# Optimization experiments

Measured on AMD Instinct MI355X. Metric: run time of the kernel, lower is better.

## Reference

```python
import jax, jax.numpy as jnp
import numpy as np

B, F, D = 16384, 40, 64  # batch, num_fields, embedding_size
D_OUT = 64               # att_embedding_size * head_num = 32 * 2


def setup_inputs() -> dict:
    key = jax.random.key(0)
    ks = jax.random.split(key, 5)
    return {
        "inputs": jax.random.normal(ks[0], (B, F, D), dtype=jnp.float32),
        "W_Query": jax.random.normal(ks[1], (D, D_OUT), dtype=jnp.float32) * 0.05,
        "W_key": jax.random.normal(ks[2], (D, D_OUT), dtype=jnp.float32) * 0.05,
        "W_Value": jax.random.normal(ks[3], (D, D_OUT), dtype=jnp.float32) * 0.05,
        "W_Res": jax.random.normal(ks[4], (D, D_OUT), dtype=jnp.float32) * 0.05,
    }


def reference(inputs, W_Query, W_key, W_Value, W_Res):
    # QKV projections (no head splitting, per original module)
    q = jnp.einsum('bfd,de->bfe', inputs, W_Query)  # [B, F, D_OUT]
    k = jnp.einsum('bfd,de->bfe', inputs, W_key)
    v = jnp.einsum('bfd,de->bfe', inputs, W_Value)
    # scaled-dot-product over the field axis; scaling=False so no divide
    scores = jax.nn.softmax(jnp.einsum('bqe,bke->bqk', q, k), axis=-1)  # [B, F, F]
    result = jnp.einsum('bqk,bke->bqe', scores, v)
    # residual projection (use_res=True)
    result = result + jnp.einsum('bfd,de->bfe', inputs, W_Res)
    return jax.nn.relu(result)
```

## Files before the change

kernel.cpp:

```cpp
#include <hip/hip_runtime.h>
#include <hip/hip_bf16.h>

#define BB  16384
#define F   40
#define LDQ 72
#define LDV 56

typedef __bf16 bf16;
typedef __bf16 bf16x8 __attribute__((ext_vector_type(8)));
typedef __bf16 bf16x4 __attribute__((ext_vector_type(4)));
typedef float  f32x4  __attribute__((ext_vector_type(4)));


__device__ __forceinline__ bf16x8 cvt8(float4 a, float4 b) {
    bf16x8 f;
    f[0] = (bf16)a.x; f[1] = (bf16)a.y; f[2] = (bf16)a.z; f[3] = (bf16)a.w;
    f[4] = (bf16)b.x; f[5] = (bf16)b.y; f[6] = (bf16)b.z; f[7] = (bf16)b.w;
    return f;
}

__global__ __launch_bounds__(256)
void prep_weights(const float* __restrict__ Wq, const float* __restrict__ Wk,
                  const float* __restrict__ Wv, const float* __restrict__ Wr,
                  bf16* __restrict__ ws)
{
    const int tid = threadIdx.x;
    if (blockIdx.x > 0) {
        const float* W = (blockIdx.x == 1) ? Wv : Wr;
        bf16* dst = ws + 4096 * blockIdx.x;
        for (int f = tid; f < 4096; f += 256) {
            int j = f & 7, ln = (f >> 3) & 63, kt = (f >> 9) & 1, nt = f >> 10;
            dst[f] = (bf16)W[(kt * 32 + (ln >> 4) * 8 + j) * 64 + nt * 16 + (ln & 15)];
        }
        return;
    }
    __shared__ float Gs[64 * 64];
    if (tid < 64) {
        const int l16 = tid & 15, quad = tid >> 4;
        bf16x8 aq[4][2], ak[4][2];
        #pragma unroll
        for (int mt = 0; mt < 4; ++mt)
            #pragma unroll
            for (int kt = 0; kt < 2; ++kt) {
                const float* pq = Wq + (mt * 16 + l16) * 64 + kt * 32 + quad * 8;
                const float* pk = Wk + (mt * 16 + l16) * 64 + kt * 32 + quad * 8;
                aq[mt][kt] = cvt8(*(const float4*)pq, *(const float4*)(pq + 4));
                ak[mt][kt] = cvt8(*(const float4*)pk, *(const float4*)(pk + 4));
            }
        #pragma unroll
        for (int mt = 0; mt < 4; ++mt)
            #pragma unroll
            for (int nt = 0; nt < 4; ++nt) {
                f32x4 acc = {0.f, 0.f, 0.f, 0.f};
                acc = __builtin_amdgcn_mfma_f32_16x16x32_bf16(aq[mt][0], ak[nt][0], acc, 0, 0, 0);
                acc = __builtin_amdgcn_mfma_f32_16x16x32_bf16(aq[mt][1], ak[nt][1], acc, 0, 0, 0);
                #pragma unroll
                for (int r = 0; r < 4; ++r)
                    Gs[(mt * 16 + quad * 4 + r) * 64 + nt * 16 + l16] = acc[r];
            }
    }
    __syncthreads();
    for (int f = tid; f < 4096; f += 256) {
        int j = f & 7, ln = (f >> 3) & 63, kt = (f >> 9) & 1, nt = f >> 10;
        ws[f] = (bf16)Gs[(kt * 32 + (ln >> 4) * 8 + j) * 64 + nt * 16 + (ln & 15)];
    }
}

__global__ __launch_bounds__(64, 3)
void attn_fused(const float* __restrict__ X, const bf16* __restrict__ wfrag,
                float* __restrict__ Out)
{
    __shared__ bf16 QB[48 * LDQ];
    __shared__ bf16 VT[64 * LDV + 8];

    const int lane = threadIdx.x;
    const int l16  = lane & 15;
    const int quad = lane >> 4;
    const int b    = blockIdx.x;
    const float* Xb = X + (size_t)b * (F * 64);

    {
        bf16x8 z = {};
        *(bf16x8*)&VT[lane * LDV + 48] = z;
        if (lane == 0) *(bf16x8*)&VT[64 * LDV] = z;
    }

    bf16x8 xf[3][2];
    #pragma unroll
    for (int mt = 0; mt < 3; ++mt) {
        int row = mt * 16 + l16; if (row >= F) row = F - 1;
        #pragma unroll
        for (int kt = 0; kt < 2; ++kt) {
            const float* p = Xb + row * 64 + kt * 32 + quad * 8;
            xf[mt][kt] = cvt8(*(const float4*)p, *(const float4*)(p + 4));
        }
    }

    const bf16x8* gF = (const bf16x8*)wfrag;
    const bf16x8* vF = gF + 512;
    const bf16x8* rF = gF + 1024;

    #pragma unroll
    for (int mt = 0; mt < 4; ++mt) {
        bf16x8 a0 = gF[(mt * 2 + 0) * 64 + lane];
        bf16x8 a1 = gF[(mt * 2 + 1) * 64 + lane];
        #pragma unroll
        for (int nt = 0; nt < 3; ++nt) {
            f32x4 acc = {0.f, 0.f, 0.f, 0.f};
            acc = __builtin_amdgcn_mfma_f32_16x16x32_bf16(a0, xf[nt][0], acc, 0, 0, 0);
            acc = __builtin_amdgcn_mfma_f32_16x16x32_bf16(a1, xf[nt][1], acc, 0, 0, 0);
            bf16x4 pk;
            pk[0] = (bf16)acc[0]; pk[1] = (bf16)acc[1];
            pk[2] = (bf16)acc[2]; pk[3] = (bf16)acc[3];
            *(bf16x4*)&QB[(nt * 16 + l16) * LDQ + mt * 16 + quad * 4] = pk;
        }
    }

    #pragma unroll
    for (int nt = 0; nt < 4; ++nt) {
        bf16x8 b0 = vF[(nt * 2 + 0) * 64 + lane];
        bf16x8 b1 = vF[(nt * 2 + 1) * 64 + lane];
        #pragma unroll
        for (int mt = 0; mt < 3; ++mt) {
            f32x4 acc = {0.f, 0.f, 0.f, 0.f};
            acc = __builtin_amdgcn_mfma_f32_16x16x32_bf16(xf[mt][0], b0, acc, 0, 0, 0);
            acc = __builtin_amdgcn_mfma_f32_16x16x32_bf16(xf[mt][1], b1, acc, 0, 0, 0);
            bf16x4 pk;
            pk[0] = (bf16)acc[0]; pk[1] = (bf16)acc[1];
            pk[2] = (bf16)acc[2]; pk[3] = (bf16)acc[3];
            *(bf16x4*)&VT[(nt * 16 + l16) * LDV + mt * 16 + quad * 4] = pk;
        }
    }

    bf16x8 qf[3][2];
    #pragma unroll
    for (int nt = 0; nt < 3; ++nt) {
        qf[nt][0] = *(const bf16x8*)&QB[(nt * 16 + l16) * LDQ + 0  + quad * 8];
        qf[nt][1] = *(const bf16x8*)&QB[(nt * 16 + l16) * LDQ + 32 + quad * 8];
    }
    f32x4 sacc[3][3];
    #pragma unroll
    for (int mt = 0; mt < 3; ++mt)
        #pragma unroll
        for (int nt = 0; nt < 3; ++nt) {
            f32x4 acc = {0.f, 0.f, 0.f, 0.f};
            acc = __builtin_amdgcn_mfma_f32_16x16x32_bf16(xf[mt][0], qf[nt][0], acc, 0, 0, 0);
            acc = __builtin_amdgcn_mfma_f32_16x16x32_bf16(xf[mt][1], qf[nt][1], acc, 0, 0, 0);
            sacc[mt][nt] = acc;
        }

    const bool dead = (quad >= 2);
    #pragma unroll
    for (int nt = 0; nt < 3; ++nt) {
        float ex[3][4]; float sum = 0.f;
        #pragma unroll
        for (int mt = 0; mt < 3; ++mt)
            #pragma unroll
            for (int r = 0; r < 4; ++r) {
                float e = (mt == 2 && dead) ? 0.f : __expf(sacc[mt][nt][r]);
                ex[mt][r] = e; sum += e;
            }
        sum += __shfl_xor(sum, 16, 64);
        sum += __shfl_xor(sum, 32, 64);
        float inv = 1.0f / sum;
        #pragma unroll
        for (int mt = 0; mt < 3; ++mt) {
            bf16x4 pk;
            pk[0] = (bf16)(ex[mt][0] * inv); pk[1] = (bf16)(ex[mt][1] * inv);
            pk[2] = (bf16)(ex[mt][2] * inv); pk[3] = (bf16)(ex[mt][3] * inv);
            *(bf16x4*)&QB[(nt * 16 + l16) * LDQ + mt * 16 + quad * 4] = pk;
        }
    }

    f32x4 oacc[4][3];
    #pragma unroll
    for (int mt = 0; mt < 4; ++mt) {
        bf16x8 a0 = rF[(mt * 2 + 0) * 64 + lane];
        bf16x8 a1 = rF[(mt * 2 + 1) * 64 + lane];
        #pragma unroll
        for (int nt = 0; nt < 3; ++nt) {
            f32x4 acc = {0.f, 0.f, 0.f, 0.f};
            acc = __builtin_amdgcn_mfma_f32_16x16x32_bf16(a0, xf[nt][0], acc, 0, 0, 0);
            acc = __builtin_amdgcn_mfma_f32_16x16x32_bf16(a1, xf[nt][1], acc, 0, 0, 0);
            oacc[mt][nt] = acc;
        }
    }
    bf16x8 ptf[3][2];
    #pragma unroll
    for (int nt = 0; nt < 3; ++nt) {
        ptf[nt][0] = *(const bf16x8*)&QB[(nt * 16 + l16) * LDQ + 0  + quad * 8];
        bf16x8 t   = *(const bf16x8*)&QB[(nt * 16 + l16) * LDQ + 32 + quad * 8];
        if (dead) t = bf16x8{};
        ptf[nt][1] = t;
    }
    #pragma unroll
    for (int mt = 0; mt < 4; ++mt) {
        bf16x8 v0 = *(const bf16x8*)&VT[(mt * 16 + l16) * LDV + 0  + quad * 8];
        bf16x8 v1 = *(const bf16x8*)&VT[(mt * 16 + l16) * LDV + 32 + quad * 8];
        #pragma unroll
        for (int nt = 0; nt < 3; ++nt) {
            f32x4 acc = oacc[mt][nt];
            acc = __builtin_amdgcn_mfma_f32_16x16x32_bf16(v0, ptf[nt][0], acc, 0, 0, 0);
            acc = __builtin_amdgcn_mfma_f32_16x16x32_bf16(v1, ptf[nt][1], acc, 0, 0, 0);
            int m = nt * 16 + l16;
            if (m < F) {
                f32x4 st;
                st[0] = fmaxf(acc[0], 0.f); st[1] = fmaxf(acc[1], 0.f);
                st[2] = fmaxf(acc[2], 0.f); st[3] = fmaxf(acc[3], 0.f);
                __builtin_nontemporal_store(st,
                    (f32x4*)&Out[(size_t)b * (F * 64) + m * 64 + mt * 16 + quad * 4]);
            }
        }
    }
}

extern "C" void kernel_launch(void* const* d_in, const int* in_sizes, int n_in,
                              void* d_out, int out_size, void* d_ws, size_t ws_size,
                              hipStream_t stream) {
    const float* X  = (const float*)d_in[0];
    const float* Wq = (const float*)d_in[1];
    const float* Wk = (const float*)d_in[2];
    const float* Wv = (const float*)d_in[3];
    const float* Wr = (const float*)d_in[4];
    float* Out = (float*)d_out;
    bf16* ws = (bf16*)d_ws;

    prep_weights<<<3, 256, 0, stream>>>(Wq, Wk, Wv, Wr, ws);
    attn_fused<<<BB, 64, 0, stream>>>(X, ws, Out);
}
```

Measured before the change: 314.2 us.

## Process four batches per block with register prefetch of next X tile

Each single-wave block now loops over four batch elements instead of one, and grid size shrinks accordingly. While the current batch is computed, the fp32 X rows for the next batch are loaded into registers so global load latency overlaps the MFMA work. The output stores are regrouped after the final accumulation. This adds register pressure from the prefetch buffer and cuts the number of blocks available to hide latency through occupancy.

```diff
diff --git a/kernel.cpp b/kernel.cpp
--- a/kernel.cpp
+++ b/kernel.cpp
@@ -3,6 +3,7 @@
 
 #define BB  16384
 #define F   40
+#define NB  4
 #define LDQ 72
 #define LDV 56
 
@@ -76,8 +77,26 @@
     const int lane = threadIdx.x;
     const int l16  = lane & 15;
     const int quad = lane >> 4;
-    const int b    = blockIdx.x;
-    const float* Xb = X + (size_t)b * (F * 64);
+    const long b0  = (long)blockIdx.x * NB;
+
+    int rowm[3];
+    #pragma unroll
+    for (int mt = 0; mt < 3; ++mt) {
+        int r = mt * 16 + l16; rowm[mt] = (r >= F) ? (F - 1) : r;
+    }
+
+    float4 xr[3][2][2];
+    {
+        const float* Xb = X + (size_t)b0 * (F * 64);
+        #pragma unroll
+        for (int mt = 0; mt < 3; ++mt)
+            #pragma unroll
+            for (int kt = 0; kt < 2; ++kt) {
+                const float* p = Xb + rowm[mt] * 64 + kt * 32 + quad * 8;
+                xr[mt][kt][0] = *(const float4*)p;
+                xr[mt][kt][1] = *(const float4*)(p + 4);
+            }
+    }
 
     {
         bf16x8 z = {};
@@ -85,130 +104,152 @@
         if (lane == 0) *(bf16x8*)&VT[64 * LDV] = z;
     }
 
-    bf16x8 xf[3][2];
-    #pragma unroll
-    for (int mt = 0; mt < 3; ++mt) {
-        int row = mt * 16 + l16; if (row >= F) row = F - 1;
-        #pragma unroll
-        for (int kt = 0; kt < 2; ++kt) {
-            const float* p = Xb + row * 64 + kt * 32 + quad * 8;
-            xf[mt][kt] = cvt8(*(const float4*)p, *(const float4*)(p + 4));
-        }
-    }
-
-    const bf16x8* gF = (const bf16x8*)wfrag;
-    const bf16x8* vF = gF + 512;
-    const bf16x8* rF = gF + 1024;
-
-    #pragma unroll
-    for (int mt = 0; mt < 4; ++mt) {
-        bf16x8 a0 = gF[(mt * 2 + 0) * 64 + lane];
-        bf16x8 a1 = gF[(mt * 2 + 1) * 64 + lane];
-        #pragma unroll
-        for (int nt = 0; nt < 3; ++nt) {
-            f32x4 acc = {0.f, 0.f, 0.f, 0.f};
-            acc = __builtin_amdgcn_mfma_f32_16x16x32_bf16(a0, xf[nt][0], acc, 0, 0, 0);
-            acc = __builtin_amdgcn_mfma_f32_16x16x32_bf16(a1, xf[nt][1], acc, 0, 0, 0);
-            bf16x4 pk;
-            pk[0] = (bf16)acc[0]; pk[1] = (bf16)acc[1];
-            pk[2] = (bf16)acc[2]; pk[3] = (bf16)acc[3];
-            *(bf16x4*)&QB[(nt * 16 + l16) * LDQ + mt * 16 + quad * 4] = pk;
-        }
-    }
-
-    #pragma unroll
-    for (int nt = 0; nt < 4; ++nt) {
-        bf16x8 b0 = vF[(nt * 2 + 0) * 64 + lane];
-        bf16x8 b1 = vF[(nt * 2 + 1) * 64 + lane];
-        #pragma unroll
-        for (int mt = 0; mt < 3; ++mt) {
-            f32x4 acc = {0.f, 0.f, 0.f, 0.f};
-            acc = __builtin_amdgcn_mfma_f32_16x16x32_bf16(xf[mt][0], b0, acc, 0, 0, 0);
-            acc = __builtin_amdgcn_mfma_f32_16x16x32_bf16(xf[mt][1], b1, acc, 0, 0, 0);
-            bf16x4 pk;
-            pk[0] = (bf16)acc[0]; pk[1] = (bf16)acc[1];
-            pk[2] = (bf16)acc[2]; pk[3] = (bf16)acc[3];
-            *(bf16x4*)&VT[(nt * 16 + l16) * LDV + mt * 16 + quad * 4] = pk;
-        }
-    }
-
-    bf16x8 qf[3][2];
-    #pragma unroll
-    for (int nt = 0; nt < 3; ++nt) {
-        qf[nt][0] = *(const bf16x8*)&QB[(nt * 16 + l16) * LDQ + 0  + quad * 8];
-        qf[nt][1] = *(const bf16x8*)&QB[(nt * 16 + l16) * LDQ + 32 + quad * 8];
-    }
-    f32x4 sacc[3][3];
-    #pragma unroll
-    for (int mt = 0; mt < 3; ++mt)
-        #pragma unroll
-        for (int nt = 0; nt < 3; ++nt) {
-            f32x4 acc = {0.f, 0.f, 0.f, 0.f};
-            acc = __builtin_amdgcn_mfma_f32_16x16x32_bf16(xf[mt][0], qf[nt][0], acc, 0, 0, 0);
-            acc = __builtin_amdgcn_mfma_f32_16x16x32_bf16(xf[mt][1], qf[nt][1], acc, 0, 0, 0);
-            sacc[mt][nt] = acc;
-        }
-
-    const bool dead = (quad >= 2);
-    #pragma unroll
-    for (int nt = 0; nt < 3; ++nt) {
-        float ex[3][4]; float sum = 0.f;
+    const bf16* wf = wfrag;
+
+    #pragma unroll 1
+    for (int i = 0; i < NB; ++i) {
+        const long b = b0 + i;
+
+        asm volatile("" : "+s"(wf));
+        const bf16x8* gF = (const bf16x8*)wf;
+        const bf16x8* vF = gF + 512;
+        const bf16x8* rF = gF + 1024;
+
+        bf16x8 xf[3][2];
         #pragma unroll
         for (int mt = 0; mt < 3; ++mt)
             #pragma unroll
-            for (int r = 0; r < 4; ++r) {
-                float e = (mt == 2 && dead) ? 0.f : __expf(sacc[mt][nt][r]);
-                ex[mt][r] = e; sum += e;
-            }
-        sum += __shfl_xor(sum, 16, 64);
-        sum += __shfl_xor(sum, 32, 64);
-        float inv = 1.0f / sum;
-        #pragma unroll
-        for (int mt = 0; mt < 3; ++mt) {
-            bf16x4 pk;
-            pk[0] = (bf16)(ex[mt][0] * inv); pk[1] = (bf16)(ex[mt][1] * inv);
-            pk[2] = (bf16)(ex[mt][2] * inv); pk[3] = (bf16)(ex[mt][3] * inv);
-            *(bf16x4*)&QB[(nt * 16 + l16) * LDQ + mt * 16 + quad * 4] = pk;
-        }
-    }
-
-    f32x4 oacc[4][3];
-    #pragma unroll
-    for (int mt = 0; mt < 4; ++mt) {
-        bf16x8 a0 = rF[(mt * 2 + 0) * 64 + lane];
-        bf16x8 a1 = rF[(mt * 2 + 1) * 64 + lane];
-        #pragma unroll
-        for (int nt = 0; nt < 3; ++nt) {
-            f32x4 acc = {0.f, 0.f, 0.f, 0.f};
-            acc = __builtin_amdgcn_mfma_f32_16x16x32_bf16(a0, xf[nt][0], acc, 0, 0, 0);
-            acc = __builtin_amdgcn_mfma_f32_16x16x32_bf16(a1, xf[nt][1], acc, 0, 0, 0);
-            oacc[mt][nt] = acc;
-        }
-    }
-    bf16x8 ptf[3][2];
-    #pragma unroll
-    for (int nt = 0; nt < 3; ++nt) {
-        ptf[nt][0] = *(const bf16x8*)&QB[(nt * 16 + l16) * LDQ + 0  + quad * 8];
-        bf16x8 t   = *(const bf16x8*)&QB[(nt * 16 + l16) * LDQ + 32 + quad * 8];
-        if (dead) t = bf16x8{};
-        ptf[nt][1] = t;
-    }
-    #pragma unroll
-    for (int mt = 0; mt < 4; ++mt) {
-        bf16x8 v0 = *(const bf16x8*)&VT[(mt * 16 + l16) * LDV + 0  + quad * 8];
-        bf16x8 v1 = *(const bf16x8*)&VT[(mt * 16 + l16) * LDV + 32 + quad * 8];
-        #pragma unroll
-        for (int nt = 0; nt < 3; ++nt) {
-            f32x4 acc = oacc[mt][nt];
-            acc = __builtin_amdgcn_mfma_f32_16x16x32_bf16(v0, ptf[nt][0], acc, 0, 0, 0);
-            acc = __builtin_amdgcn_mfma_f32_16x16x32_bf16(v1, ptf[nt][1], acc, 0, 0, 0);
+            for (int kt = 0; kt < 2; ++kt)
+                xf[mt][kt] = cvt8(xr[mt][kt][0], xr[mt][kt][1]);
+
+        if (i + 1 < NB) {
+            const float* Xn = X + (size_t)(b + 1) * (F * 64);
+            #pragma unroll
+            for (int mt = 0; mt < 3; ++mt)
+                #pragma unroll
+                for (int kt = 0; kt < 2; ++kt) {
+                    const float* p = Xn + rowm[mt] * 64 + kt * 32 + quad * 8;
+                    xr[mt][kt][0] = *(const float4*)p;
+                    xr[mt][kt][1] = *(const float4*)(p + 4);
+                }
+        }
+
+        #pragma unroll
+        for (int mt = 0; mt < 4; ++mt) {
+            bf16x8 a0 = gF[(mt * 2 + 0) * 64 + lane];
+            bf16x8 a1 = gF[(mt * 2 + 1) * 64 + lane];
+            #pragma unroll
+            for (int nt = 0; nt < 3; ++nt) {
+                f32x4 acc = {0.f, 0.f, 0.f, 0.f};
+                acc = __builtin_amdgcn_mfma_f32_16x16x32_bf16(a0, xf[nt][0], acc, 0, 0, 0);
+                acc = __builtin_amdgcn_mfma_f32_16x16x32_bf16(a1, xf[nt][1], acc, 0, 0, 0);
+                bf16x4 pk;
+                pk[0] = (bf16)acc[0]; pk[1] = (bf16)acc[1];
+                pk[2] = (bf16)acc[2]; pk[3] = (bf16)acc[3];
+                *(bf16x4*)&QB[(nt * 16 + l16) * LDQ + mt * 16 + quad * 4] = pk;
+            }
+        }
+
+        #pragma unroll
+        for (int nt = 0; nt < 4; ++nt) {
+            bf16x8 bw0 = vF[(nt * 2 + 0) * 64 + lane];
+            bf16x8 bw1 = vF[(nt * 2 + 1) * 64 + lane];
+            #pragma unroll
+            for (int mt = 0; mt < 3; ++mt) {
+                f32x4 acc = {0.f, 0.f, 0.f, 0.f};
+                acc = __builtin_amdgcn_mfma_f32_16x16x32_bf16(xf[mt][0], bw0, acc, 0, 0, 0);
+                acc = __builtin_amdgcn_mfma_f32_16x16x32_bf16(xf[mt][1], bw1, acc, 0, 0, 0);
+                bf16x4 pk;
+                pk[0] = (bf16)acc[0]; pk[1] = (bf16)acc[1];
+                pk[2] = (bf16)acc[2]; pk[3] = (bf16)acc[3];
+                *(bf16x4*)&VT[(nt * 16 + l16) * LDV + mt * 16 + quad * 4] = pk;
+            }
+        }
+
+        bf16x8 qf[3][2];
+        #pragma unroll
+        for (int nt = 0; nt < 3; ++nt) {
+            qf[nt][0] = *(const bf16x8*)&QB[(nt * 16 + l16) * LDQ + 0  + quad * 8];
+            qf[nt][1] = *(const bf16x8*)&QB[(nt * 16 + l16) * LDQ + 32 + quad * 8];
+        }
+        f32x4 sacc[3][3];
+        #pragma unroll
+        for (int mt = 0; mt < 3; ++mt)
+            #pragma unroll
+            for (int nt = 0; nt < 3; ++nt) {
+                f32x4 acc = {0.f, 0.f, 0.f, 0.f};
+                acc = __builtin_amdgcn_mfma_f32_16x16x32_bf16(xf[mt][0], qf[nt][0], acc, 0, 0, 0);
+                acc = __builtin_amdgcn_mfma_f32_16x16x32_bf16(xf[mt][1], qf[nt][1], acc, 0, 0, 0);
+                sacc[mt][nt] = acc;
+            }
+
+        const bool dead = (quad >= 2);
+        #pragma unroll
+        for (int nt = 0; nt < 3; ++nt) {
+            float ex[3][4]; float sum = 0.f;
+            #pragma unroll
+            for (int mt = 0; mt < 3; ++mt)
+                #pragma unroll
+                for (int r = 0; r < 4; ++r) {
+                    float e = (mt == 2 && dead) ? 0.f : __expf(sacc[mt][nt][r]);
+                    ex[mt][r] = e; sum += e;
+                }
+            sum += __shfl_xor(sum, 16, 64);
+            sum += __shfl_xor(sum, 32, 64);
+            float inv = 1.0f / sum;
+            #pragma unroll
+            for (int mt = 0; mt < 3; ++mt) {
+                bf16x4 pk;
+                pk[0] = (bf16)(ex[mt][0] * inv); pk[1] = (bf16)(ex[mt][1] * inv);
+                pk[2] = (bf16)(ex[mt][2] * inv); pk[3] = (bf16)(ex[mt][3] * inv);
+                *(bf16x4*)&QB[(nt * 16 + l16) * LDQ + mt * 16 + quad * 4] = pk;
+            }
+        }
+
+        f32x4 oacc[4][3];
+        #pragma unroll
+        for (int mt = 0; mt < 4; ++mt) {
+            bf16x8 a0 = rF[(mt * 2 + 0) * 64 + lane];
+            bf16x8 a1 = rF[(mt * 2 + 1) * 64 + lane];
+            #pragma unroll
+            for (int nt = 0; nt < 3; ++nt) {
+                f32x4 acc = {0.f, 0.f, 0.f, 0.f};
+                acc = __builtin_amdgcn_mfma_f32_16x16x32_bf16(a0, xf[nt][0], acc, 0, 0, 0);
+                acc = __builtin_amdgcn_mfma_f32_16x16x32_bf16(a1, xf[nt][1], acc, 0, 0, 0);
+                oacc[mt][nt] = acc;
+            }
+        }
+        bf16x8 ptf[3][2];
+        #pragma unroll
+        for (int nt = 0; nt < 3; ++nt) {
+            ptf[nt][0] = *(const bf16x8*)&QB[(nt * 16 + l16) * LDQ + 0  + quad * 8];
+            bf16x8 t   = *(const bf16x8*)&QB[(nt * 16 + l16) * LDQ + 32 + quad * 8];
+            if (dead) t = bf16x8{};
+            ptf[nt][1] = t;
+        }
+        #pragma unroll
+        for (int mt = 0; mt < 4; ++mt) {
+            bf16x8 v0 = *(const bf16x8*)&VT[(mt * 16 + l16) * LDV + 0  + quad * 8];
+            bf16x8 v1 = *(const bf16x8*)&VT[(mt * 16 + l16) * LDV + 32 + quad * 8];
+            #pragma unroll
+            for (int nt = 0; nt < 3; ++nt) {
+                oacc[mt][nt] = __builtin_amdgcn_mfma_f32_16x16x32_bf16(v0, ptf[nt][0], oacc[mt][nt], 0, 0, 0);
+                oacc[mt][nt] = __builtin_amdgcn_mfma_f32_16x16x32_bf16(v1, ptf[nt][1], oacc[mt][nt], 0, 0, 0);
+            }
+        }
+        float* Ob = Out + (size_t)b * (F * 64);
+        #pragma unroll
+        for (int nt = 0; nt < 3; ++nt) {
             int m = nt * 16 + l16;
             if (m < F) {
-                f32x4 st;
-                st[0] = fmaxf(acc[0], 0.f); st[1] = fmaxf(acc[1], 0.f);
-                st[2] = fmaxf(acc[2], 0.f); st[3] = fmaxf(acc[3], 0.f);
-                __builtin_nontemporal_store(st,
-                    (f32x4*)&Out[(size_t)b * (F * 64) + m * 64 + mt * 16 + quad * 4]);
+                #pragma unroll
+                for (int mt = 0; mt < 4; ++mt) {
+                    f32x4 st;
+                    st[0] = fmaxf(oacc[mt][nt][0], 0.f); st[1] = fmaxf(oacc[mt][nt][1], 0.f);
+                    st[2] = fmaxf(oacc[mt][nt][2], 0.f); st[3] = fmaxf(oacc[mt][nt][3], 0.f);
+                    __builtin_nontemporal_store(st,
+                        (f32x4*)&Ob[m * 64 + mt * 16 + quad * 4]);
+                }
             }
         }
     }
@@ -226,5 +267,5 @@
     bf16* ws = (bf16*)d_ws;
 
     prep_weights<<<3, 256, 0, stream>>>(Wq, Wk, Wv, Wr, ws);
-    attn_fused<<<BB, 64, 0, stream>>>(X, ws, Out);
-}
+    attn_fused<<<BB / NB, 64, 0, stream>>>(X, ws, Out);
+}
```

Result: slower. 335.8 us (+6.9%).

## Eliminate shared memory by chaining MFMA outputs as 16x16x16 operands in registers

Applied to the files above, without the earlier changes.

Drops the LDS staging buffers for Q, V and the softmax probabilities. MFMA accumulator outputs are packed to bf16x4 and fed straight into 16x16x16 bf16 MFMAs as operands, relying on the C/D register layout matching the A/B operand layout of that instruction. X is also reloaded in a second 4-wide fragment layout, and the residual and output accumulation is split into two halves to limit live registers. Occupancy hint rises from 3 to 4 waves. It trades LDS traffic for twice as many half-width MFMAs and extra global reloads of X. The higher occupancy target may also cause register spills.

```diff
diff --git a/kernel.cpp b/kernel.cpp
--- a/kernel.cpp
+++ b/kernel.cpp
@@ -3,12 +3,11 @@
 
 #define BB  16384
 #define F   40
-#define LDQ 72
-#define LDV 56
 
 typedef __bf16 bf16;
 typedef __bf16 bf16x8 __attribute__((ext_vector_type(8)));
 typedef __bf16 bf16x4 __attribute__((ext_vector_type(4)));
+typedef short  s16x4  __attribute__((ext_vector_type(4)));
 typedef float  f32x4  __attribute__((ext_vector_type(4)));
 
 
@@ -17,6 +16,27 @@
     f[0] = (bf16)a.x; f[1] = (bf16)a.y; f[2] = (bf16)a.z; f[3] = (bf16)a.w;
     f[4] = (bf16)b.x; f[5] = (bf16)b.y; f[6] = (bf16)b.z; f[7] = (bf16)b.w;
     return f;
+}
+__device__ __forceinline__ bf16x4 cvt4(float4 a) {
+    bf16x4 f;
+    f[0] = (bf16)a.x; f[1] = (bf16)a.y; f[2] = (bf16)a.z; f[3] = (bf16)a.w;
+    return f;
+}
+__device__ __forceinline__ bf16x4 pack4(f32x4 a) {
+    bf16x4 f;
+    f[0] = (bf16)a[0]; f[1] = (bf16)a[1]; f[2] = (bf16)a[2]; f[3] = (bf16)a[3];
+    return f;
+}
+__device__ __forceinline__ f32x4 mfma32(bf16x8 a, bf16x8 b, f32x4 c) {
+    return __builtin_amdgcn_mfma_f32_16x16x32_bf16(a, b, c, 0, 0, 0);
+}
+__device__ __forceinline__ f32x4 mfma16(bf16x4 a, bf16x4 b, f32x4 c) {
+#if __has_builtin(__builtin_amdgcn_mfma_f32_16x16x16_bf16)
+    return __builtin_amdgcn_mfma_f32_16x16x16_bf16(a, b, c, 0, 0, 0);
+#else
+    return __builtin_amdgcn_mfma_f32_16x16x16bf16_1k(
+        __builtin_bit_cast(s16x4, a), __builtin_bit_cast(s16x4, b), c, 0, 0, 0);
+#endif
 }
 
 __global__ __launch_bounds__(256)
@@ -52,8 +72,8 @@
             #pragma unroll
             for (int nt = 0; nt < 4; ++nt) {
                 f32x4 acc = {0.f, 0.f, 0.f, 0.f};
-                acc = __builtin_amdgcn_mfma_f32_16x16x32_bf16(aq[mt][0], ak[nt][0], acc, 0, 0, 0);
-                acc = __builtin_amdgcn_mfma_f32_16x16x32_bf16(aq[mt][1], ak[nt][1], acc, 0, 0, 0);
+                acc = mfma32(aq[mt][0], ak[nt][0], acc);
+                acc = mfma32(aq[mt][1], ak[nt][1], acc);
                 #pragma unroll
                 for (int r = 0; r < 4; ++r)
                     Gs[(mt * 16 + quad * 4 + r) * 64 + nt * 16 + l16] = acc[r];
@@ -66,40 +86,44 @@
     }
 }
 
-__global__ __launch_bounds__(64, 3)
+__global__ __launch_bounds__(64, 4)
 void attn_fused(const float* __restrict__ X, const bf16* __restrict__ wfrag,
                 float* __restrict__ Out)
 {
-    __shared__ bf16 QB[48 * LDQ];
-    __shared__ bf16 VT[64 * LDV + 8];
-
     const int lane = threadIdx.x;
     const int l16  = lane & 15;
     const int quad = lane >> 4;
-    const int b    = blockIdx.x;
-    const float* Xb = X + (size_t)b * (F * 64);
-
-    {
-        bf16x8 z = {};
-        *(bf16x8*)&VT[lane * LDV + 48] = z;
-        if (lane == 0) *(bf16x8*)&VT[64 * LDV] = z;
+    const float* Xb = X + (size_t)blockIdx.x * (F * 64);
+
+    int rowm[3];
+    #pragma unroll
+    for (int mt = 0; mt < 3; ++mt) {
+        int r = mt * 16 + l16; rowm[mt] = (r >= F) ? (F - 1) : r;
     }
 
     bf16x8 xf[3][2];
     #pragma unroll
-    for (int mt = 0; mt < 3; ++mt) {
-        int row = mt * 16 + l16; if (row >= F) row = F - 1;
+    for (int mt = 0; mt < 3; ++mt)
         #pragma unroll
         for (int kt = 0; kt < 2; ++kt) {
-            const float* p = Xb + row * 64 + kt * 32 + quad * 8;
+            const float* p = Xb + rowm[mt] * 64 + kt * 32 + quad * 8;
             xf[mt][kt] = cvt8(*(const float4*)p, *(const float4*)(p + 4));
         }
-    }
+
+    bf16x4 xa[3][4];
+    #pragma unroll
+    for (int mt = 0; mt < 3; ++mt)
+        #pragma unroll
+        for (int kt = 0; kt < 4; ++kt) {
+            const float* p = Xb + rowm[mt] * 64 + kt * 16 + quad * 4;
+            xa[mt][kt] = cvt4(*(const float4*)p);
+        }
 
     const bf16x8* gF = (const bf16x8*)wfrag;
     const bf16x8* vF = gF + 512;
     const bf16x8* rF = gF + 1024;
 
+    bf16x4 pkQ[4][3];
     #pragma unroll
     for (int mt = 0; mt < 4; ++mt) {
         bf16x8 a0 = gF[(mt * 2 + 0) * 64 + lane];
@@ -107,49 +131,26 @@
         #pragma unroll
         for (int nt = 0; nt < 3; ++nt) {
             f32x4 acc = {0.f, 0.f, 0.f, 0.f};
-            acc = __builtin_amdgcn_mfma_f32_16x16x32_bf16(a0, xf[nt][0], acc, 0, 0, 0);
-            acc = __builtin_amdgcn_mfma_f32_16x16x32_bf16(a1, xf[nt][1], acc, 0, 0, 0);
-            bf16x4 pk;
-            pk[0] = (bf16)acc[0]; pk[1] = (bf16)acc[1];
-            pk[2] = (bf16)acc[2]; pk[3] = (bf16)acc[3];
-            *(bf16x4*)&QB[(nt * 16 + l16) * LDQ + mt * 16 + quad * 4] = pk;
-        }
-    }
-
-    #pragma unroll
-    for (int nt = 0; nt < 4; ++nt) {
-        bf16x8 b0 = vF[(nt * 2 + 0) * 64 + lane];
-        bf16x8 b1 = vF[(nt * 2 + 1) * 64 + lane];
-        #pragma unroll
-        for (int mt = 0; mt < 3; ++mt) {
-            f32x4 acc = {0.f, 0.f, 0.f, 0.f};
-            acc = __builtin_amdgcn_mfma_f32_16x16x32_bf16(xf[mt][0], b0, acc, 0, 0, 0);
-            acc = __builtin_amdgcn_mfma_f32_16x16x32_bf16(xf[mt][1], b1, acc, 0, 0, 0);
-            bf16x4 pk;
-            pk[0] = (bf16)acc[0]; pk[1] = (bf16)acc[1];
-            pk[2] = (bf16)acc[2]; pk[3] = (bf16)acc[3];
-            *(bf16x4*)&VT[(nt * 16 + l16) * LDV + mt * 16 + quad * 4] = pk;
-        }
-    }
-
-    bf16x8 qf[3][2];
-    #pragma unroll
-    for (int nt = 0; nt < 3; ++nt) {
-        qf[nt][0] = *(const bf16x8*)&QB[(nt * 16 + l16) * LDQ + 0  + quad * 8];
-        qf[nt][1] = *(const bf16x8*)&QB[(nt * 16 + l16) * LDQ + 32 + quad * 8];
-    }
+            acc = mfma32(a0, xf[nt][0], acc);
+            acc = mfma32(a1, xf[nt][1], acc);
+            pkQ[mt][nt] = pack4(acc);
+        }
+    }
+
     f32x4 sacc[3][3];
     #pragma unroll
     for (int mt = 0; mt < 3; ++mt)
         #pragma unroll
         for (int nt = 0; nt < 3; ++nt) {
             f32x4 acc = {0.f, 0.f, 0.f, 0.f};
-            acc = __builtin_amdgcn_mfma_f32_16x16x32_bf16(xf[mt][0], qf[nt][0], acc, 0, 0, 0);
-            acc = __builtin_amdgcn_mfma_f32_16x16x32_bf16(xf[mt][1], qf[nt][1], acc, 0, 0, 0);
+            #pragma unroll
+            for (int kt = 0; kt < 4; ++kt)
+                acc = mfma16(xa[mt][kt], pkQ[kt][nt], acc);
             sacc[mt][nt] = acc;
         }
 
     const bool dead = (quad >= 2);
+    bf16x4 pkP[3][3];
     #pragma unroll
     for (int nt = 0; nt < 3; ++nt) {
         float ex[3][4]; float sum = 0.f;
@@ -168,47 +169,65 @@
             bf16x4 pk;
             pk[0] = (bf16)(ex[mt][0] * inv); pk[1] = (bf16)(ex[mt][1] * inv);
             pk[2] = (bf16)(ex[mt][2] * inv); pk[3] = (bf16)(ex[mt][3] * inv);
-            *(bf16x4*)&QB[(nt * 16 + l16) * LDQ + mt * 16 + quad * 4] = pk;
-        }
-    }
-
-    f32x4 oacc[4][3];
-    #pragma unroll
-    for (int mt = 0; mt < 4; ++mt) {
-        bf16x8 a0 = rF[(mt * 2 + 0) * 64 + lane];
-        bf16x8 a1 = rF[(mt * 2 + 1) * 64 + lane];
+            pkP[mt][nt] = pk;
+        }
+    }
+
+    bf16x4 pkV[3][4];
+    #pragma unroll
+    for (int nt = 0; nt < 4; ++nt) {
+        bf16x8 b0 = vF[(nt * 2 + 0) * 64 + lane];
+        bf16x8 b1 = vF[(nt * 2 + 1) * 64 + lane];
+        #pragma unroll
+        for (int mt = 0; mt < 3; ++mt) {
+            f32x4 acc = {0.f, 0.f, 0.f, 0.f};
+            acc = mfma32(xf[mt][0], b0, acc);
+            acc = mfma32(xf[mt][1], b1, acc);
+            pkV[mt][nt] = pack4(acc);
+        }
+    }
+
+    float* Ob = Out + (size_t)blockIdx.x * (F * 64);
+    #pragma unroll
+    for (int half = 0; half < 2; ++half) {
+        f32x4 oacc[2][3];
+        #pragma unroll
+        for (int me = 0; me < 2; ++me) {
+            int mt = half * 2 + me;
+            bf16x8 a0 = rF[(mt * 2 + 0) * 64 + lane];
+            bf16x8 a1 = rF[(mt * 2 + 1) * 64 + lane];
+            #pragma unroll
+            for (int nt = 0; nt < 3; ++nt) {
+                f32x4 acc = {0.f, 0.f, 0.f, 0.f};
+                acc = mfma32(a0, xf[nt][0], acc);
+                acc = mfma32(a1, xf[nt][1], acc);
+                oacc[me][nt] = acc;
+            }
+        }
+        #pragma unroll
+        for (int me = 0; me < 2; ++me) {
+            int mt = half * 2 + me;
+            #pragma unroll
+            for (int nt = 0; nt < 3; ++nt) {
+                f32x4 acc = oacc[me][nt];
+                #pragma unroll
+                for (int kt = 0; kt < 3; ++kt)
+                    acc = mfma16(pkV[kt][mt], pkP[kt][nt], acc);
+                oacc[me][nt] = acc;
+            }
+        }
         #pragma unroll
         for (int nt = 0; nt < 3; ++nt) {
-            f32x4 acc = {0.f, 0.f, 0.f, 0.f};
-            acc = __builtin_amdgcn_mfma_f32_16x16x32_bf16(a0, xf[nt][0], acc, 0, 0, 0);
-            acc = __builtin_amdgcn_mfma_f32_16x16x32_bf16(a1, xf[nt][1], acc, 0, 0, 0);
-            oacc[mt][nt] = acc;
-        }
-    }
-    bf16x8 ptf[3][2];
-    #pragma unroll
-    for (int nt = 0; nt < 3; ++nt) {
-        ptf[nt][0] = *(const bf16x8*)&QB[(nt * 16 + l16) * LDQ + 0  + quad * 8];
-        bf16x8 t   = *(const bf16x8*)&QB[(nt * 16 + l16) * LDQ + 32 + quad * 8];
-        if (dead) t = bf16x8{};
-        ptf[nt][1] = t;
-    }
-    #pragma unroll
-    for (int mt = 0; mt < 4; ++mt) {
-        bf16x8 v0 = *(const bf16x8*)&VT[(mt * 16 + l16) * LDV + 0  + quad * 8];
-        bf16x8 v1 = *(const bf16x8*)&VT[(mt * 16 + l16) * LDV + 32 + quad * 8];
-        #pragma unroll
-        for (int nt = 0; nt < 3; ++nt) {
-            f32x4 acc = oacc[mt][nt];
-            acc = __builtin_amdgcn_mfma_f32_16x16x32_bf16(v0, ptf[nt][0], acc, 0, 0, 0);
-            acc = __builtin_amdgcn_mfma_f32_16x16x32_bf16(v1, ptf[nt][1], acc, 0, 0, 0);
             int m = nt * 16 + l16;
             if (m < F) {
-                f32x4 st;
-                st[0] = fmaxf(acc[0], 0.f); st[1] = fmaxf(acc[1], 0.f);
-                st[2] = fmaxf(acc[2], 0.f); st[3] = fmaxf(acc[3], 0.f);
-                __builtin_nontemporal_store(st,
-                    (f32x4*)&Out[(size_t)b * (F * 64) + m * 64 + mt * 16 + quad * 4]);
+                #pragma unroll
+                for (int me = 0; me < 2; ++me) {
+                    f32x4 st;
+                    st[0] = fmaxf(oacc[me][nt][0], 0.f); st[1] = fmaxf(oacc[me][nt][1], 0.f);
+                    st[2] = fmaxf(oacc[me][nt][2], 0.f); st[3] = fmaxf(oacc[me][nt][3], 0.f);
+                    __builtin_nontemporal_store(st,
+                        (f32x4*)&Ob[m * 64 + (half * 2 + me) * 16 + quad * 4]);
+                }
             }
         }
     }
```

After: 333.8 us. 6.2% more time.
